# Kernel tuning notes

Hardware: AMD Instinct MI355X
Metric: run time of the kernel (lower is better)

## Reference

```python
import jax, jax.numpy as jnp
import numpy as np

N = 30000   # nodes
E = 480000  # edges
IN = 128    # hidden_dim (in_feats)
H = 4       # num_heads
D = 128     # out_feats per head
HD = H * D
NEG_SLOPE = 0.2
BN_EPS = 1e-5


def setup_inputs() -> dict:
    key = jax.random.key(0)
    ks = jax.random.split(key, 12)
    feat = jax.random.normal(ks[0], (N, IN), dtype=jnp.float32)
    src = jax.random.randint(ks[1], (E,), 0, N)
    dst = jax.random.randint(ks[2], (E,), 0, N)
    sc_in = 1.0 / np.sqrt(IN)
    sc_hd = 1.0 / np.sqrt(HD)
    W_fc = jax.random.normal(ks[3], (IN, HD), dtype=jnp.float32) * sc_in
    attn_l = jax.random.normal(ks[4], (H, D), dtype=jnp.float32) * sc_in
    attn_r = jax.random.normal(ks[5], (H, D), dtype=jnp.float32) * sc_in
    W_res = jax.random.normal(ks[6], (IN, HD), dtype=jnp.float32) * sc_in
    bias_gat = jnp.zeros((HD,), dtype=jnp.float32)
    gamma = jnp.ones((HD,), dtype=jnp.float32)
    beta = jnp.zeros((HD,), dtype=jnp.float32)
    W_out = jax.random.normal(ks[7], (HD, IN), dtype=jnp.float32) * sc_hd
    b_out = jnp.zeros((IN,), dtype=jnp.float32)
    return dict(feat=feat, src=src, dst=dst, W_fc=W_fc, attn_l=attn_l,
                attn_r=attn_r, W_res=W_res, bias_gat=bias_gat,
                gamma=gamma, beta=beta, W_out=W_out, b_out=b_out)


def reference(feat, src, dst, W_fc, attn_l, attn_r, W_res, bias_gat,
              gamma, beta, W_out, b_out):
    # --- GATConv (eval mode: dropout off) ---
    h = (feat @ W_fc).reshape(N, H, D)               # projected feats [N,H,D]
    el = jnp.einsum('nhd,hd->nh', h, attn_l)         # [N,H]
    er = jnp.einsum('nhd,hd->nh', h, attn_r)         # [N,H]
    e = el[src] + er[dst]                            # [E,H]
    e = jnp.where(e > 0, e, NEG_SLOPE * e)           # leaky_relu(0.2)
    # segment softmax over edges grouped by destination node
    emax = jax.ops.segment_max(e, dst, num_segments=N)   # [N,H]
    emax = jnp.where(jnp.isfinite(emax), emax, 0.0)      # empty segments
    ex = jnp.exp(e - emax[dst])                          # [E,H]
    denom = jax.ops.segment_sum(ex, dst, num_segments=N) # [N,H]
    a = ex / denom[dst]                                  # [E,H] attention
    msgs = h[src] * a[:, :, None]                        # [E,H,D]
    rst = jax.ops.segment_sum(msgs, dst, num_segments=N) # [N,H,D]
    # residual (in_feats != H*out_feats -> linear res_fc) + bias
    rst = rst + (feat @ W_res).reshape(N, H, D) + bias_gat.reshape(1, H, D)
    # --- fc_out: Flatten -> BatchNorm1d (train stats) -> ReLU -> Linear ---
    x = rst.reshape(N, HD)
    mu = x.mean(axis=0)
    var = x.var(axis=0)
    xn = (x - mu) / jnp.sqrt(var + BN_EPS)
    x = jnp.maximum(gamma * xn + beta, 0.0)
    return x @ W_out + b_out                             # [N, IN]
```

## Files before the change

kernel.cpp:

```cpp
#include <hip/hip_runtime.h>

#define N_  30000
#define E_  480000

typedef short short8 __attribute__((ext_vector_type(8)));
typedef float f32x4  __attribute__((ext_vector_type(4)));
typedef float f32x2  __attribute__((ext_vector_type(2)));
typedef unsigned int u32x4 __attribute__((ext_vector_type(4)));
typedef unsigned int u32x2 __attribute__((ext_vector_type(2)));
typedef int i32x4 __attribute__((ext_vector_type(4)));
union Frag { u32x4 q; short8 v; unsigned short us[8]; };

__device__ __forceinline__ float b2f(unsigned short u){
  union { unsigned int i; float f; } v; v.i = ((unsigned int)u) << 16; return v.f;
}
__device__ __forceinline__ float blo(unsigned int u){
  union { unsigned int i; float f; } v; v.i = u << 16; return v.f;
}
__device__ __forceinline__ float bhi(unsigned int u){
  union { unsigned int i; float f; } v; v.i = u & 0xffff0000u; return v.f;
}
__device__ __forceinline__ unsigned short f2b(float f){
  union { float f; unsigned int u; } v; v.f = f;
  unsigned int u = v.u;
  return (unsigned short)((u + 0x7fffu + ((u >> 16) & 1u)) >> 16);
}
__device__ __forceinline__ void gl_lds16(const unsigned short* g, unsigned short* l){
  __builtin_amdgcn_global_load_lds(
      (const __attribute__((address_space(1))) unsigned int*)g,
      (__attribute__((address_space(3))) unsigned int*)l, 16, 0, 0);
}

__global__ void k_initconv(const float* __restrict__ Wfc, const float* __restrict__ Wres,
                           const float* __restrict__ Wout,
                           const float* __restrict__ al, const float* __restrict__ ar,
                           unsigned short* __restrict__ Wt2s, unsigned short* __restrict__ WtOuts,
                           float* __restrict__ P,
                           int* __restrict__ counts, int* __restrict__ cursor){
  int bx = blockIdx.x;
  if (bx >= 256){
    int idx = (bx - 256) * 256 + threadIdx.x;
    if (idx < 1024){
      int k = idx >> 3, q = idx & 7;
      int h = q & 3;
      const float* a = (q < 4) ? al : ar;
      const float* wr = Wfc + k * 512 + h * 128;
      const float* av = a + h * 128;
      float s = 0.f;
#pragma unroll 4
      for (int d = 0; d < 128; d++) s += wr[d] * av[d];
      P[k * 8 + q] = s;
    }
    return;
  }
  int gid = bx * 256 + threadIdx.x;
  const int stride = 256 * 256;
  if (gid < N_){ counts[gid] = 0; cursor[gid] = 0; }
  const int total1 = 131072;
  const int total2 = 65536;
  for (int i = gid; i < total1 + total2; i += stride){
    if (i < total1){
      int tile = i >> 14, E = i & 16383;
      int ph = tile >> 2, by = tile & 3;
      int col = E >> 7, remE = E & 127;
      int unit = (remE >> 3) ^ (col & 7);
      int k = unit * 8 + (remE & 7);
      int c = by * 128 + col;
      float v = ph ? Wres[k * 512 + c] : Wfc[k * 512 + c];
      Wt2s[i] = f2b(v);
    } else {
      int j = i - total1;
      int ph = j >> 14, E = j & 16383;
      int col = E >> 7, remE = E & 127;
      int unit = (remE >> 3) ^ (col & 7);
      int k = unit * 8 + (remE & 7);
      WtOuts[j] = f2b(Wout[(ph * 128 + k) * 128 + col]);
    }
  }
}

__global__ __launch_bounds__(256) void k_el(const float* __restrict__ feat,
                                            const float* __restrict__ P,
                                            float* __restrict__ el, float* __restrict__ er,
                                            unsigned short* __restrict__ featb){
  __shared__ float sF[32 * 132];
  __shared__ float sP[1024];
  int t = threadIdx.x;
  int n0 = blockIdx.x * 32;
  *reinterpret_cast<f32x4*>(&sP[t * 4]) = *reinterpret_cast<const f32x4*>(P + t * 4);
#pragma unroll
  for (int i = 0; i < 4; i++){
    int c = t + i * 256;
    int r = c >> 5, cw = (c & 31) * 4;
    int gn = n0 + r;
    f32x4 v = {0.f, 0.f, 0.f, 0.f};
    if (gn < N_) v = *reinterpret_cast<const f32x4*>(feat + gn * 128 + cw);
    *reinterpret_cast<f32x4*>(&sF[r * 132 + cw]) = v;
  }
  __syncthreads();
#pragma unroll
  for (int i = 0; i < 8; i++){
    int c = t + i * 256;
    int r = c >> 6, cw = (c & 63) * 2;
    int gn = n0 + r;
    if (gn < N_){
      float v0 = sF[r * 132 + cw], v1 = sF[r * 132 + cw + 1];
      unsigned int pv = (unsigned int)f2b(v0) | ((unsigned int)f2b(v1) << 16);
      *reinterpret_cast<unsigned int*>(featb + gn * 128 + cw) = pv;
    }
  }
  int node = t >> 3, q = t & 7;
  int gn = n0 + node;
  const float* fr = &sF[node * 132];
  float s = 0.f;
#pragma unroll 2
  for (int k = 0; k < 128; k += 4){
    f32x4 fv = *reinterpret_cast<const f32x4*>(fr + k);
#pragma unroll
    for (int j = 0; j < 4; j++) s += fv[j] * sP[(k + j) * 8 + q];
  }
  if (gn < N_){
    if (q < 4) el[gn * 4 + q] = s;
    else       er[gn * 4 + (q - 4)] = s;
  }
}

__global__ void k_hist(const int* __restrict__ dst, int* __restrict__ counts){
  int e = blockIdx.x * 256 + threadIdx.x;
  if (e < E_) atomicAdd(&counts[dst[e]], 1);
}

__global__ __launch_bounds__(1024) void k_scan(const int* __restrict__ counts,
                                               int* __restrict__ offs){
  __shared__ int wsum[16];
  int t = threadIdx.x;
  int lane = t & 63, w = t >> 6;
  int base = t * 32;
  int vals[32];
  int s = 0;
  bool inb = (base < N_);
#pragma unroll
  for (int jj = 0; jj < 8; jj++){
    i32x4 cv = {0, 0, 0, 0};
    if (inb) cv = *reinterpret_cast<const i32x4*>(counts + base + jj * 4);
#pragma unroll
    for (int m = 0; m < 4; m++){
      int idx = base + jj * 4 + m;
      int v = (idx < N_) ? cv[m] : 0;
      vals[jj * 4 + m] = s;
      s += v;
    }
  }
  int x = s;
  for (int o = 1; o < 64; o <<= 1){
    int y = __shfl_up(x, o);
    if (lane >= o) x += y;
  }
  if (lane == 63) wsum[w] = x;
  __syncthreads();
  if (t < 16){
    int y = wsum[t];
    for (int o = 1; o < 16; o <<= 1){
      int z = __shfl_up(y, o, 16);
      if (t >= o) y += z;
    }
    wsum[t] = y;
  }
  __syncthreads();
  int wbase = (w > 0) ? wsum[w - 1] : 0;
  int ex = wbase + x - s;
#pragma unroll
  for (int j = 0; j < 32; j++){
    int idx = base + j;
    if (idx <= N_) offs[idx] = ex + vals[j];
  }
}

__global__ void k_edge(const int* __restrict__ src, const int* __restrict__ dst,
                       const float* __restrict__ el, const float* __restrict__ er,
                       float* __restrict__ ws_s, int* __restrict__ src_s,
                       const int* __restrict__ offs, int* __restrict__ cursor){
  int e = blockIdx.x * 256 + threadIdx.x;
  if (e >= E_) return;
  int s = src[e], d = dst[e];
  f32x4 a = *reinterpret_cast<const f32x4*>(el + s * 4);
  f32x4 b = *reinterpret_cast<const f32x4*>(er + d * 4);
  f32x4 v;
#pragma unroll
  for (int i = 0; i < 4; i++){
    float x = a[i] + b[i];
    x = x > 0.f ? x : 0.2f * x;
    v[i] = __expf(x);
  }
  int p = atomicAdd(&cursor[d], 1);
  int pos = offs[d] + p;
  *reinterpret_cast<f32x4*>(ws_s + pos * 4) = v;
  src_s[pos] = s;
}

__global__ __launch_bounds__(256) void k_aggrf(const int* __restrict__ offs,
                                               const int* __restrict__ src_s,
                                               const float* __restrict__ ws_s,
                                               const unsigned short* __restrict__ featb,
                                               unsigned short* __restrict__ fagg){
  int wave = threadIdx.x >> 6, lane = threadIdx.x & 63;
  int n = blockIdx.x * 4 + wave;
  if (n >= N_) return;
  int off0 = __builtin_amdgcn_readfirstlane(offs[n]);
  int g    = __builtin_amdgcn_readfirstlane(offs[n + 1]) - off0;
  int c0 = lane * 2;
  f32x2 acc2[4] = {};
  f32x4 wsum = {0.f, 0.f, 0.f, 0.f};

  auto FMA1 = [&](const f32x4& wv, unsigned int pv){
    wsum += wv;
    f32x2 lh; lh[0] = blo(pv); lh[1] = bhi(pv);
#pragma unroll
    for (int h = 0; h < 4; h++) acc2[h] += lh * wv[h];
  };

  int i = 0;
  while (i < g){
    int blk = g - i; if (blk > 64) blk = 64;
    int idx = i + lane;
    int ssrc = (idx < g) ? src_s[off0 + idx] : 0;
    int nfull = blk >> 3;
    if (nfull){
      int sa[8]; unsigned int pa[8]; f32x4 wa[8];
#pragma unroll
      for (int u = 0; u < 8; u++) sa[u] = __shfl(ssrc, u);
#pragma unroll
      for (int u = 0; u < 8; u++) pa[u] = *reinterpret_cast<const unsigned int*>(featb + sa[u] * 128 + c0);
#pragma unroll
      for (int u = 0; u < 8; u++) wa[u] = *reinterpret_cast<const f32x4*>(ws_s + (off0 + i + u) * 4);
      for (int c = 1; c < nfull; c++){
        int sb[8]; unsigned int pb[8]; f32x4 wb[8];
#pragma unroll
        for (int u = 0; u < 8; u++) sb[u] = __shfl(ssrc, c * 8 + u);
#pragma unroll
        for (int u = 0; u < 8; u++) pb[u] = *reinterpret_cast<const unsigned int*>(featb + sb[u] * 128 + c0);
#pragma unroll
        for (int u = 0; u < 8; u++) wb[u] = *reinterpret_cast<const f32x4*>(ws_s + (off0 + i + c * 8 + u) * 4);
#pragma unroll
        for (int u = 0; u < 8; u++) FMA1(wa[u], pa[u]);
#pragma unroll
        for (int u = 0; u < 8; u++){ pa[u] = pb[u]; wa[u] = wb[u]; }
      }
#pragma unroll
      for (int u = 0; u < 8; u++) FMA1(wa[u], pa[u]);
    }
    for (int j = nfull * 8; j < blk; j++){
      int s = __shfl(ssrc, j);
      unsigned int pv = *reinterpret_cast<const unsigned int*>(featb + s * 128 + c0);
      f32x4 wv = *reinterpret_cast<const f32x4*>(ws_s + (off0 + i + j) * 4);
      FMA1(wv, pv);
    }
    i += blk;
  }

  f32x4 rd;
#pragma unroll
  for (int h = 0; h < 4; h++) rd[h] = (wsum[h] > 0.f) ? 1.0f / wsum[h] : 0.f;
#pragma unroll
  for (int h = 0; h < 4; h++){
    unsigned int ov = (unsigned int)f2b(acc2[h][0] * rd[h]) |
                      ((unsigned int)f2b(acc2[h][1] * rd[h]) << 16);
    *reinterpret_cast<unsigned int*>(fagg + n * 512 + h * 128 + c0) = ov;
  }
}

__global__ __launch_bounds__(512) void k_gemmC(const unsigned short* __restrict__ fagg,
                                               const unsigned short* __restrict__ featb,
                                               const unsigned short* __restrict__ Wt2s,
                                               const float* __restrict__ bias,
                                               unsigned short* __restrict__ comb){
  __shared__ unsigned short wsl[128 * 128];
  char* wb = (char*)wsl;
  int tid = threadIdx.x;
  int wave = tid >> 6, lane = tid & 63;
  int lrow = lane & 15, quad = lane >> 4;
  int rowbase = blockIdx.x * 128 + wave * 16;
  int colbase = blockIdx.y * 128;
  int arow = rowbase + lrow; if (arow > N_ - 1) arow = N_ - 1;
  const unsigned short* aF = fagg + arow * 512 + colbase;
  const unsigned short* aX = featb + arow * 128;
  f32x4 acc[8] = {};
  for (int phase = 0; phase < 2; phase++){
    __syncthreads();
    {
      const unsigned short* gt = Wt2s + (((phase << 2) | (int)blockIdx.y) << 14);
#pragma unroll
      for (int i = 0; i < 4; i++){
        int off = ((i << 3) | wave) << 9;
        gl_lds16(gt + off + (lane << 3), wsl + off);
      }
    }
    __syncthreads();
#pragma unroll
    for (int kk = 0; kk < 4; kk++){
      Frag a;
      a.q = (phase == 0)
          ? *reinterpret_cast<const u32x4*>(aF + kk * 32 + quad * 8)
          : *reinterpret_cast<const u32x4*>(aX + kk * 32 + quad * 8);
#pragma unroll
      for (int s = 0; s < 8; s++){
        int r = s * 16 + lrow;
        int byte = (r * 256 + kk * 64 + quad * 16) ^ ((r & 7) << 4);
        Frag b; b.q = *reinterpret_cast<const u32x4*>(wb + byte);
        acc[s] = __builtin_amdgcn_mfma_f32_16x16x32_bf16(b.v, a.v, acc[s], 0, 0, 0);
      }
    }
  }
  int gr = rowbase + lrow;
  if (gr < N_){
    unsigned short* crow = comb + gr * 512 + colbase;
#pragma unroll
    for (int s = 0; s < 8; s++){
      f32x4 bb = *reinterpret_cast<const f32x4*>(bias + colbase + s * 16 + quad * 4);
      u32x2 ov;
#pragma unroll
      for (int d = 0; d < 2; d++){
        float v0 = acc[s][2 * d]     + bb[2 * d];
        float v1 = acc[s][2 * d + 1] + bb[2 * d + 1];
        ov[d] = (unsigned int)f2b(v0) | ((unsigned int)f2b(v1) << 16);
      }
      *reinterpret_cast<u32x2*>(crow + s * 16 + quad * 4) = ov;
    }
  }
}

__global__ __launch_bounds__(256) void k_stats(const unsigned short* __restrict__ comb,
                                               float* __restrict__ psum,
                                               float* __restrict__ psq){
  __shared__ float lsum[4][512];
  __shared__ float lsq[4][512];
  int t = threadIdx.x, lane = t & 63, rg = t >> 6;
  int c0 = lane * 8;
  const int rows = 118;
  int r0 = blockIdx.x * rows;
  int r1 = r0 + rows; if (r1 > N_) r1 = N_;
  float s[8] = {}, q[8] = {};
  for (int r = r0 + rg; r < r1; r += 4){
    u32x4 pv = *reinterpret_cast<const u32x4*>(comb + r * 512 + c0);
#pragma unroll
    for (int d = 0; d < 4; d++){
      float v0 = blo(pv[d]);
      float v1 = bhi(pv[d]);
      s[2*d]   += v0; q[2*d]   += v0 * v0;
      s[2*d+1] += v1; q[2*d+1] += v1 * v1;
    }
  }
#pragma unroll
  for (int d = 0; d < 8; d++){ lsum[rg][c0 + d] = s[d]; lsq[rg][c0 + d] = q[d]; }
  __syncthreads();
#pragma unroll
  for (int half = 0; half < 2; half++){
    int ch = t + half * 256;
    float a = lsum[0][ch] + lsum[1][ch] + lsum[2][ch] + lsum[3][ch];
    float b = lsq[0][ch] + lsq[1][ch] + lsq[2][ch] + lsq[3][ch];
    psum[blockIdx.x * 512 + ch] = a;
    psq[blockIdx.x * 512 + ch] = b;
  }
}

__global__ __launch_bounds__(128) void k_bnfin(const float* __restrict__ psum,
                                               const float* __restrict__ psq,
                                               const float* __restrict__ gamma,
                                               const float* __restrict__ beta,
                                               float* __restrict__ scale,
                                               float* __restrict__ shift){
  int ch = blockIdx.x * 128 + threadIdx.x;
  float s0 = 0.f, s1 = 0.f, s2 = 0.f, s3 = 0.f;
  float q0 = 0.f, q1 = 0.f, q2 = 0.f, q3 = 0.f;
  for (int b = 0; b < 256; b += 4){
    s0 += psum[(b    ) * 512 + ch];
    s1 += psum[(b + 1) * 512 + ch];
    s2 += psum[(b + 2) * 512 + ch];
    s3 += psum[(b + 3) * 512 + ch];
    q0 += psq[(b    ) * 512 + ch];
    q1 += psq[(b + 1) * 512 + ch];
    q2 += psq[(b + 2) * 512 + ch];
    q3 += psq[(b + 3) * 512 + ch];
  }
  float sum = (s0 + s1) + (s2 + s3);
  float sq  = (q0 + q1) + (q2 + q3);
  float mu  = sum / (float)N_;
  float var = sq / (float)N_ - mu * mu;
  float inv = rsqrtf(var + 1e-5f);
  float sc  = gamma[ch] * inv;
  scale[ch] = sc;
  shift[ch] = beta[ch] - mu * sc;
}

__global__ __launch_bounds__(256) void k_gemm2(const unsigned short* __restrict__ comb,
                                               const unsigned short* __restrict__ WtOuts,
                                               const float* __restrict__ scale,
                                               const float* __restrict__ shift,
                                               const float* __restrict__ bout,
                                               float* __restrict__ out){
  __shared__ float sc[512], sh[512];
  __shared__ unsigned short wsl[128 * 128];
  char* wb = (char*)wsl;
  int t = threadIdx.x;
  for (int i = t; i < 512; i += 256){ sc[i] = scale[i]; sh[i] = shift[i]; }
  int wave = t >> 6, lane = t & 63, lrow = lane & 15, quad = lane >> 4;
  int rowbase = blockIdx.x * 64 + wave * 16;
  int rr = rowbase + lrow; if (rr > N_ - 1) rr = N_ - 1;
  const unsigned short* arow = comb + rr * 512;
  f32x4 acc[8] = {};
  for (int phase = 0; phase < 4; phase++){
    __syncthreads();
    {
      const unsigned short* gt = WtOuts + (phase << 14);
#pragma unroll
      for (int i = 0; i < 8; i++){
        int off = ((i << 2) | wave) << 9;
        gl_lds16(gt + off + (lane << 3), wsl + off);
      }
    }
    __syncthreads();
#pragma unroll
    for (int kk = 0; kk < 4; kk++){
      int base = phase * 128 + kk * 32 + quad * 8;
      Frag a; a.q = *reinterpret_cast<const u32x4*>(arow + base);
#pragma unroll
      for (int i2 = 0; i2 < 8; i2++){
        float x = b2f(a.us[i2]);
        x = fmaf(x, sc[base + i2], sh[base + i2]);
        a.us[i2] = f2b(fmaxf(x, 0.0f));
      }
#pragma unroll
      for (int s = 0; s < 8; s++){
        int r = s * 16 + lrow;
        int byte = (r * 256 + kk * 64 + quad * 16) ^ ((r & 7) << 4);
        Frag b; b.q = *reinterpret_cast<const u32x4*>(wb + byte);
        acc[s] = __builtin_amdgcn_mfma_f32_16x16x32_bf16(b.v, a.v, acc[s], 0, 0, 0);
      }
    }
  }
  int gr = rowbase + lrow;
  if (gr < N_){
    float* orow = out + gr * 128;
#pragma unroll
    for (int s = 0; s < 8; s++){
      int cb = s * 16 + quad * 4;
      f32x4 bb = *reinterpret_cast<const f32x4*>(bout + cb);
      f32x4 ov;
#pragma unroll
      for (int j = 0; j < 4; j++) ov[j] = acc[s][j] + bb[j];
      *reinterpret_cast<f32x4*>(orow + cb) = ov;
    }
  }
}

extern "C" void kernel_launch(void* const* d_in, const int* in_sizes, int n_in,
                              void* d_out, int out_size, void* d_ws, size_t ws_size,
                              hipStream_t stream){
  const float* feat  = (const float*)d_in[0];
  const int*   src   = (const int*)d_in[1];
  const int*   dst   = (const int*)d_in[2];
  const float* Wfc   = (const float*)d_in[3];
  const float* al    = (const float*)d_in[4];
  const float* ar    = (const float*)d_in[5];
  const float* Wres  = (const float*)d_in[6];
  const float* bias  = (const float*)d_in[7];
  const float* gamma = (const float*)d_in[8];
  const float* beta  = (const float*)d_in[9];
  const float* Wout  = (const float*)d_in[10];
  const float* bout  = (const float*)d_in[11];
  float* out = (float*)d_out;

  char* ws = (char*)d_ws;
  unsigned short* comb  = (unsigned short*)(ws + 0);
  unsigned short* fagg  = (unsigned short*)(ws + 30720000);
  unsigned short* Wt2s  = (unsigned short*)(ws + 61440000);
  unsigned short* WtOuts= (unsigned short*)(ws + 61702144);
  float*          el    = (float*)(ws + 61833216);
  float*          er    = (float*)(ws + 62313216);
  float*          ws_s  = (float*)(ws + 62793216);
  int*            offs  = (int*)(ws + 70473216);
  int*            counts= (int*)(ws + 70593280);
  int*            cursor= (int*)(ws + 70713280);
  int*            src_s = (int*)(ws + 70833280);
  float*          psum  = (float*)(ws + 72753280);
  float*          psq   = (float*)(ws + 73277568);
  float*          scale = (float*)(ws + 73801856);
  float*          shift = (float*)(ws + 73803904);
  unsigned short* featb = (unsigned short*)(ws + 73805952);
  float*          P     = psum;

  k_initconv<<<260, 256, 0, stream>>>(Wfc, Wres, Wout, al, ar, Wt2s, WtOuts, P,
                                      counts, cursor);
  k_hist<<<(E_ + 255) / 256, 256, 0, stream>>>(dst, counts);
  k_scan<<<1, 1024, 0, stream>>>(counts, offs);
  k_el<<<(N_ + 31) / 32, 256, 0, stream>>>(feat, P, el, er, featb);
  k_edge<<<(E_ + 255) / 256, 256, 0, stream>>>(src, dst, el, er, ws_s, src_s, offs, cursor);
  k_aggrf<<<(N_ + 3) / 4, 256, 0, stream>>>(offs, src_s, ws_s, featb, fagg);
  dim3 gC((N_ + 127) / 128, 4);
  k_gemmC<<<gC, 512, 0, stream>>>(fagg, featb, Wt2s, bias, comb);
  k_stats<<<256, 256, 0, stream>>>(comb, psum, psq);
  k_bnfin<<<4, 128, 0, stream>>>(psum, psq, gamma, beta, scale, shift);
  k_gemm2<<<(N_ + 63) / 64, 256, 0, stream>>>(comb, WtOuts, scale, shift, bout, out);
}
```

Measured before the change: 259.9 us.

## Fuse histogram into el kernel, split node aggregation across two waves, widen stats grid

Merges the destination-degree histogram and the el/er projection into one launch, with separate block ranges for each job, which removes a kernel launch. The aggregation kernel now gives each node two waves that each handle half of its edges, then combines the partial sums through shared memory to raise parallelism on the latency-bound gather. The BN stats kernel doubles its block count with half the rows per block and reuses a freed workspace region for the partial sums. The cost is a block-wide barrier in aggregation, and blocks of the fused kernel doing unrelated work.

```diff
diff --git a/kernel.cpp b/kernel.cpp
--- a/kernel.cpp
+++ b/kernel.cpp
@@ -79,14 +79,22 @@
   }
 }
 
-__global__ __launch_bounds__(256) void k_el(const float* __restrict__ feat,
-                                            const float* __restrict__ P,
-                                            float* __restrict__ el, float* __restrict__ er,
-                                            unsigned short* __restrict__ featb){
+__global__ __launch_bounds__(256) void k_elhist(const float* __restrict__ feat,
+                                                const float* __restrict__ P,
+                                                const int* __restrict__ dst,
+                                                int* __restrict__ counts,
+                                                float* __restrict__ el, float* __restrict__ er,
+                                                unsigned short* __restrict__ featb){
   __shared__ float sF[32 * 132];
   __shared__ float sP[1024];
+  int bx = blockIdx.x;
+  if (bx < 1875){
+    int e = bx * 256 + threadIdx.x;
+    if (e < E_) atomicAdd(&counts[dst[e]], 1);
+    return;
+  }
   int t = threadIdx.x;
-  int n0 = blockIdx.x * 32;
+  int n0 = (bx - 1875) * 32;
   *reinterpret_cast<f32x4*>(&sP[t * 4]) = *reinterpret_cast<const f32x4*>(P + t * 4);
 #pragma unroll
   for (int i = 0; i < 4; i++){
@@ -123,11 +131,6 @@
     if (q < 4) el[gn * 4 + q] = s;
     else       er[gn * 4 + (q - 4)] = s;
   }
-}
-
-__global__ void k_hist(const int* __restrict__ dst, int* __restrict__ counts){
-  int e = blockIdx.x * 256 + threadIdx.x;
-  if (e < E_) atomicAdd(&counts[dst[e]], 1);
 }
 
 __global__ __launch_bounds__(1024) void k_scan(const int* __restrict__ counts,
@@ -203,11 +206,15 @@
                                                const float* __restrict__ ws_s,
                                                const unsigned short* __restrict__ featb,
                                                unsigned short* __restrict__ fagg){
+  __shared__ float red[4][64][8];
+  __shared__ float wsr[4][4];
   int wave = threadIdx.x >> 6, lane = threadIdx.x & 63;
-  int n = blockIdx.x * 4 + wave;
-  if (n >= N_) return;
+  int n = blockIdx.x * 2 + (wave >> 1);
+  int half = wave & 1;
   int off0 = __builtin_amdgcn_readfirstlane(offs[n]);
   int g    = __builtin_amdgcn_readfirstlane(offs[n + 1]) - off0;
+  int e0 = half ? (g >> 1) : 0;
+  int e1 = half ? g : (g >> 1);
   int c0 = lane * 2;
   f32x2 acc2[4] = {};
   f32x4 wsum = {0.f, 0.f, 0.f, 0.f};
@@ -219,11 +226,11 @@
     for (int h = 0; h < 4; h++) acc2[h] += lh * wv[h];
   };
 
-  int i = 0;
-  while (i < g){
-    int blk = g - i; if (blk > 64) blk = 64;
+  int i = e0;
+  while (i < e1){
+    int blk = e1 - i; if (blk > 64) blk = 64;
     int idx = i + lane;
-    int ssrc = (idx < g) ? src_s[off0 + idx] : 0;
+    int ssrc = (idx < e1) ? src_s[off0 + idx] : 0;
     int nfull = blk >> 3;
     if (nfull){
       int sa[8]; unsigned int pa[8]; f32x4 wa[8];
@@ -258,14 +265,29 @@
     i += blk;
   }
 
-  f32x4 rd;
-#pragma unroll
-  for (int h = 0; h < 4; h++) rd[h] = (wsum[h] > 0.f) ? 1.0f / wsum[h] : 0.f;
-#pragma unroll
-  for (int h = 0; h < 4; h++){
-    unsigned int ov = (unsigned int)f2b(acc2[h][0] * rd[h]) |
-                      ((unsigned int)f2b(acc2[h][1] * rd[h]) << 16);
-    *reinterpret_cast<unsigned int*>(fagg + n * 512 + h * 128 + c0) = ov;
+  f32x4 lo = {acc2[0][0], acc2[0][1], acc2[1][0], acc2[1][1]};
+  f32x4 hi = {acc2[2][0], acc2[2][1], acc2[3][0], acc2[3][1]};
+  *reinterpret_cast<f32x4*>(&red[wave][lane][0]) = lo;
+  *reinterpret_cast<f32x4*>(&red[wave][lane][4]) = hi;
+  if (lane == 0) *reinterpret_cast<f32x4*>(&wsr[wave][0]) = wsum;
+  __syncthreads();
+  if (half == 0){
+    f32x4 pa = *reinterpret_cast<const f32x4*>(&red[wave + 1][lane][0]);
+    f32x4 pb = *reinterpret_cast<const f32x4*>(&red[wave + 1][lane][4]);
+    acc2[0][0] += pa[0]; acc2[0][1] += pa[1];
+    acc2[1][0] += pa[2]; acc2[1][1] += pa[3];
+    acc2[2][0] += pb[0]; acc2[2][1] += pb[1];
+    acc2[3][0] += pb[2]; acc2[3][1] += pb[3];
+    wsum += *reinterpret_cast<const f32x4*>(&wsr[wave + 1][0]);
+    f32x4 rd;
+#pragma unroll
+    for (int h = 0; h < 4; h++) rd[h] = (wsum[h] > 0.f) ? 1.0f / wsum[h] : 0.f;
+#pragma unroll
+    for (int h = 0; h < 4; h++){
+      unsigned int ov = (unsigned int)f2b(acc2[h][0] * rd[h]) |
+                        ((unsigned int)f2b(acc2[h][1] * rd[h]) << 16);
+      *reinterpret_cast<unsigned int*>(fagg + n * 512 + h * 128 + c0) = ov;
+    }
   }
 }
 
@@ -336,7 +358,7 @@
   __shared__ float lsq[4][512];
   int t = threadIdx.x, lane = t & 63, rg = t >> 6;
   int c0 = lane * 8;
-  const int rows = 118;
+  const int rows = 59;
   int r0 = blockIdx.x * rows;
   int r1 = r0 + rows; if (r1 > N_) r1 = N_;
   float s[8] = {}, q[8] = {};
@@ -372,7 +394,7 @@
   int ch = blockIdx.x * 128 + threadIdx.x;
   float s0 = 0.f, s1 = 0.f, s2 = 0.f, s3 = 0.f;
   float q0 = 0.f, q1 = 0.f, q2 = 0.f, q3 = 0.f;
-  for (int b = 0; b < 256; b += 4){
+  for (int b = 0; b < 512; b += 4){
     s0 += psum[(b    ) * 512 + ch];
     s1 += psum[(b + 1) * 512 + ch];
     s2 += psum[(b + 2) * 512 + ch];
@@ -482,23 +504,23 @@
   int*            counts= (int*)(ws + 70593280);
   int*            cursor= (int*)(ws + 70713280);
   int*            src_s = (int*)(ws + 70833280);
-  float*          psum  = (float*)(ws + 72753280);
-  float*          psq   = (float*)(ws + 73277568);
+  float*          Pbuf  = (float*)(ws + 72753280);
   float*          scale = (float*)(ws + 73801856);
   float*          shift = (float*)(ws + 73803904);
   unsigned short* featb = (unsigned short*)(ws + 73805952);
-  float*          P     = psum;
-
-  k_initconv<<<260, 256, 0, stream>>>(Wfc, Wres, Wout, al, ar, Wt2s, WtOuts, P,
+  float*          psumS = (float*)(ws + 62793216);
+  float*          psqS  = (float*)(ws + 63841792);
+
+  k_initconv<<<260, 256, 0, stream>>>(Wfc, Wres, Wout, al, ar, Wt2s, WtOuts, Pbuf,
                                       counts, cursor);
-  k_hist<<<(E_ + 255) / 256, 256, 0, stream>>>(dst, counts);
+  k_elhist<<<1875 + (N_ + 31) / 32, 256, 0, stream>>>(feat, Pbuf, dst, counts,
+                                                      el, er, featb);
   k_scan<<<1, 1024, 0, stream>>>(counts, offs);
-  k_el<<<(N_ + 31) / 32, 256, 0, stream>>>(feat, P, el, er, featb);
   k_edge<<<(E_ + 255) / 256, 256, 0, stream>>>(src, dst, el, er, ws_s, src_s, offs, cursor);
-  k_aggrf<<<(N_ + 3) / 4, 256, 0, stream>>>(offs, src_s, ws_s, featb, fagg);
+  k_aggrf<<<N_ / 2, 256, 0, stream>>>(offs, src_s, ws_s, featb, fagg);
   dim3 gC((N_ + 127) / 128, 4);
   k_gemmC<<<gC, 512, 0, stream>>>(fagg, featb, Wt2s, bias, comb);
-  k_stats<<<256, 256, 0, stream>>>(comb, psum, psq);
-  k_bnfin<<<4, 128, 0, stream>>>(psum, psq, gamma, beta, scale, shift);
+  k_stats<<<512, 256, 0, stream>>>(comb, psumS, psqS);
+  k_bnfin<<<4, 128, 0, stream>>>(psumS, psqS, gamma, beta, scale, shift);
   k_gemm2<<<(N_ + 63) / 64, 256, 0, stream>>>(comb, WtOuts, scale, shift, bout, out);
 }
```

New measurement: 285.2 us. 9.7% more time.
